# Optimization experiments

Hardware: AMD Instinct MI355X
Metric: run time of the kernel (lower is better)

## Reference

```python
import jax, jax.numpy as jnp
import numpy as np

MAX_DISP = 4  # pad_size == max_displacement per module validation
EPS = 1e-12   # torch F.normalize default eps


def _l2_normalize(x):
    # F.normalize(x) with default dim=1 (channels), p=2
    norm = jnp.sqrt(jnp.sum(x * x, axis=1, keepdims=True))
    return x / jnp.maximum(norm, EPS)


def setup_inputs() -> dict:
    key = jax.random.key(0)
    k1, k2 = jax.random.split(key)
    B, C, H, W = 8, 256, 96, 128
    fr = jax.random.normal(k1, (B, C, H, W), dtype=jnp.float32)
    fq = jax.random.normal(k2, (B, C, H, W), dtype=jnp.float32)
    return {"fr": fr, "fq": fq}


def reference(fr, fq):
    r = MAX_DISP
    H, W = fr.shape[2], fr.shape[3]
    frn = _l2_normalize(fr)
    # Normalization is per-pixel over channels, so normalize-then-pad equals
    # pad-then-normalize (padded zero columns stay zero under the eps clamp).
    fq_pad = jnp.pad(_l2_normalize(fq), ((0, 0), (0, 0), (r, r), (r, r)))
    # Offset order: dy (rows) outer, dx (cols) inner -> matches torch meshgrid 'ij' flatten.
    outs = [
        jnp.mean(frn * fq_pad[:, :, dy:H + dy, dx:W + dx], axis=1, keepdims=True)
        for dy in range(2 * r + 1)
        for dx in range(2 * r + 1)
    ]
    return jnp.concatenate(outs, axis=1)  # (B, (2r+1)^2, H, W)
```

## Files before the change

### kernel.cpp

```cpp
#include <hip/hip_runtime.h>


#define BB 8
#define CC 256
#define HH 96
#define WW 128
#define HW (HH*WW)
#define CHW (CC*HW)
#define NDISP 81
#define TYS 4
#define HX4 18
#define NSLOT (TYS*HX4)
#define CK 4
#define NCHK (CC/CK)
#define NST (NSLOT*CK)
#define YT (HH/TYS)
#define XT 2
#define NTILES (BB*YT*XT)
#define NGRP 9
#define EPSN 1e-12f

__device__ __forceinline__ void dma16(const void* g, void* l) {
    __builtin_amdgcn_global_load_lds(
        (const __attribute__((address_space(1))) void*)g,
        (__attribute__((address_space(3))) void*)l,
        16, 0, 0);
}

__global__ __launch_bounds__(64) __attribute__((amdgpu_waves_per_eu(4, 4)))
void corr_kernel(
    const float* __restrict__ fr, const float* __restrict__ fq,
    float* __restrict__ out)
{
    __shared__ float4 s_fq[2][NST];

    const int lane = threadIdx.x;
    const int tx   = lane & 15;
    const int ty   = lane >> 4;

    const int tile = blockIdx.x % NTILES;
    const int dy   = blockIdx.x / NTILES;
    const int b    = tile / (YT * XT);
    const int rem  = tile % (YT * XT);
    const int y0   = (rem >> 1) * TYS;
    const int x0   = (rem & 1) * 64;

    int soff[5];
#pragma unroll
    for (int j = 0; j < 5; ++j) {
        int i = 64 * j + lane;
        int c    = (i / NSLOT) & 3;
        int s    = i % NSLOT;
        int row  = s / HX4;
        int col4 = s % HX4;
        int gy = y0 + dy - 4 + row;
        int gx = x0 - 4 + col4 * 4;
        gy = min(max(gy, 0), HH - 1);
        gx = min(max(gx, 0), WW - 4);
        soff[j] = b * CHW + c * HW + gy * WW + gx;
    }

    const int frbase = b * CHW + (y0 + ty) * WW + x0 + tx * 4;

#pragma unroll
    for (int j = 0; j < 4; ++j)
        dma16(fq + soff[j], &s_fq[0][64 * j]);
    if (lane < 32)
        dma16(fq + soff[4], &s_fq[0][256]);

    float4 fra[CK];
#pragma unroll
    for (int c = 0; c < CK; ++c)
        fra[c] = *(const float4*)(fr + frbase + c * HW);

    float4 acc[9];
#pragma unroll
    for (int d = 0; d < 9; ++d) acc[d] = make_float4(0.f, 0.f, 0.f, 0.f);
    float sqn[12];
#pragma unroll
    for (int i = 0; i < 12; ++i) sqn[i] = 0.f;
    float4 fr2 = make_float4(0.f, 0.f, 0.f, 0.f);

#pragma unroll 1
    for (int ch = 0; ch < NCHK; ++ch) {
        const int p   = ch & 1;
        const int nch = (ch + 1 < NCHK) ? ch + 1 : ch;
        const int nco = nch * (CK * HW);

#pragma unroll
        for (int j = 0; j < 4; ++j)
            dma16(fq + soff[j] + nco, &s_fq[1 - p][64 * j]);
        if (lane < 32)
            dma16(fq + soff[4] + nco, &s_fq[1 - p][256]);

        __builtin_amdgcn_s_waitcnt(0x0F79);
        __builtin_amdgcn_sched_barrier(0);

#pragma unroll
        for (int c = 0; c < CK; ++c) {
            float4 a = fra[c];
            fra[c] = *(const float4*)(fr + frbase + nco + c * HW);
            fr2.x += a.x * a.x; fr2.y += a.y * a.y;
            fr2.z += a.z * a.z; fr2.w += a.w * a.w;

            float rw[12];
#pragma unroll
            for (int s4 = 0; s4 < 3; ++s4) {
                float4 t = s_fq[p][c * NSLOT + ty * HX4 + tx + s4];
                rw[s4 * 4 + 0] = t.x;
                rw[s4 * 4 + 1] = t.y;
                rw[s4 * 4 + 2] = t.z;
                rw[s4 * 4 + 3] = t.w;
            }
#pragma unroll
            for (int i = 0; i < 12; ++i) sqn[i] += rw[i] * rw[i];
#pragma unroll
            for (int dx = 0; dx < 9; ++dx) {
                acc[dx].x += a.x * rw[dx + 0];
                acc[dx].y += a.y * rw[dx + 1];
                acc[dx].z += a.z * rw[dx + 2];
                acc[dx].w += a.w * rw[dx + 3];
            }
        }
    }

    __builtin_amdgcn_s_waitcnt(0x0F70);

    float inq[12];
#pragma unroll
    for (int i = 0; i < 12; ++i)
        inq[i] = 1.0f / fmaxf(sqrtf(sqn[i]), EPSN);

    float4 ir;
    ir.x = 1.0f / fmaxf(sqrtf(fr2.x), EPSN);
    ir.y = 1.0f / fmaxf(sqrtf(fr2.y), EPSN);
    ir.z = 1.0f / fmaxf(sqrtf(fr2.z), EPSN);
    ir.w = 1.0f / fmaxf(sqrtf(fr2.w), EPSN);

    const bool rowok = ((unsigned)(y0 + ty + dy - 4) < (unsigned)HH);
    const int  xe0   = x0 + tx * 4;
    const float inv256 = 1.0f / 256.0f;
    const int obase = (b * NDISP + dy * 9) * HW + (y0 + ty) * WW + xe0;
#pragma unroll
    for (int dx = 0; dx < 9; ++dx) {
        float4 a = acc[dx];
        float4 o;
        o.x = a.x * ir.x * inq[dx + 0] * inv256;
        o.y = a.y * ir.y * inq[dx + 1] * inv256;
        o.z = a.z * ir.z * inq[dx + 2] * inv256;
        o.w = a.w * ir.w * inq[dx + 3] * inv256;
        const int cb = xe0 + dx - 4;
        o.x = (rowok && (unsigned)(cb    ) < (unsigned)WW) ? o.x : 0.f;
        o.y = (rowok && (unsigned)(cb + 1) < (unsigned)WW) ? o.y : 0.f;
        o.z = (rowok && (unsigned)(cb + 2) < (unsigned)WW) ? o.z : 0.f;
        o.w = (rowok && (unsigned)(cb + 3) < (unsigned)WW) ? o.w : 0.f;
        *(float4*)(out + obase + dx * HW) = o;
    }
}

extern "C" void kernel_launch(void* const* d_in, const int* in_sizes, int n_in,
                              void* d_out, int out_size, void* d_ws, size_t ws_size,
                              hipStream_t stream) {
    const float* fr = (const float*)d_in[0];
    const float* fq = (const float*)d_in[1];
    float* out = (float*)d_out;
    corr_kernel<<<dim3(NTILES * NGRP), dim3(64), 0, stream>>>(fr, fq, out);
}
```

Measured before the change: 326.8 us.

## Process three vertical displacements per block sharing a taller fq halo tile

```diff
diff --git a/kernel.cpp b/kernel.cpp
--- a/kernel.cpp
+++ b/kernel.cpp
@@ -9,15 +9,18 @@
 #define CHW (CC*HW)
 #define NDISP 81
 #define TYS 4
+#define GD 3
+#define HROWS (TYS+GD-1)
 #define HX4 18
-#define NSLOT (TYS*HX4)
+#define NSLOT (HROWS*HX4)
 #define CK 4
+#define CKHW (CK*HW)
 #define NCHK (CC/CK)
 #define NST (NSLOT*CK)
 #define YT (HH/TYS)
 #define XT 2
 #define NTILES (BB*YT*XT)
-#define NGRP 9
+#define NGRP 3
 #define EPSN 1e-12f
 
 __device__ __forceinline__ void dma16(const void* g, void* l) {
@@ -27,7 +30,7 @@
         16, 0, 0);
 }
 
-__global__ __launch_bounds__(64) __attribute__((amdgpu_waves_per_eu(4, 4)))
+__global__ __launch_bounds__(64) __attribute__((amdgpu_waves_per_eu(2, 8)))
 void corr_kernel(
     const float* __restrict__ fr, const float* __restrict__ fq,
     float* __restrict__ out)
@@ -39,21 +42,21 @@
     const int ty   = lane >> 4;
 
     const int tile = blockIdx.x % NTILES;
-    const int dy   = blockIdx.x / NTILES;
+    const int dyg  = blockIdx.x / NTILES;
     const int b    = tile / (YT * XT);
     const int rem  = tile % (YT * XT);
     const int y0   = (rem >> 1) * TYS;
     const int x0   = (rem & 1) * 64;
 
-    int soff[5];
+    int soff[7];
 #pragma unroll
-    for (int j = 0; j < 5; ++j) {
+    for (int j = 0; j < 7; ++j) {
         int i = 64 * j + lane;
         int c    = (i / NSLOT) & 3;
         int s    = i % NSLOT;
         int row  = s / HX4;
         int col4 = s % HX4;
-        int gy = y0 + dy - 4 + row;
+        int gy = y0 + 3 * dyg - 4 + row;
         int gx = x0 - 4 + col4 * 4;
         gy = min(max(gy, 0), HH - 1);
         gx = min(max(gx, 0), WW - 4);
@@ -63,37 +66,41 @@
     const int frbase = b * CHW + (y0 + ty) * WW + x0 + tx * 4;
 
 #pragma unroll
-    for (int j = 0; j < 4; ++j)
+    for (int j = 0; j < 6; ++j)
         dma16(fq + soff[j], &s_fq[0][64 * j]);
-    if (lane < 32)
-        dma16(fq + soff[4], &s_fq[0][256]);
+    if (lane < 48)
+        dma16(fq + soff[6], &s_fq[0][384]);
 
     float4 fra[CK];
 #pragma unroll
     for (int c = 0; c < CK; ++c)
         fra[c] = *(const float4*)(fr + frbase + c * HW);
 
-    float4 acc[9];
+    float4 acc[GD][9];
 #pragma unroll
-    for (int d = 0; d < 9; ++d) acc[d] = make_float4(0.f, 0.f, 0.f, 0.f);
-    float sqn[12];
+    for (int g = 0; g < GD; ++g)
 #pragma unroll
-    for (int i = 0; i < 12; ++i) sqn[i] = 0.f;
+        for (int d = 0; d < 9; ++d) acc[g][d] = make_float4(0.f, 0.f, 0.f, 0.f);
+    float sqn[GD][12];
+#pragma unroll
+    for (int g = 0; g < GD; ++g)
+#pragma unroll
+        for (int i = 0; i < 12; ++i) sqn[g][i] = 0.f;
     float4 fr2 = make_float4(0.f, 0.f, 0.f, 0.f);
 
 #pragma unroll 1
     for (int ch = 0; ch < NCHK; ++ch) {
         const int p   = ch & 1;
         const int nch = (ch + 1 < NCHK) ? ch + 1 : ch;
-        const int nco = nch * (CK * HW);
+        const int nco = nch * CKHW;
 
 #pragma unroll
-        for (int j = 0; j < 4; ++j)
+        for (int j = 0; j < 6; ++j)
             dma16(fq + soff[j] + nco, &s_fq[1 - p][64 * j]);
-        if (lane < 32)
-            dma16(fq + soff[4] + nco, &s_fq[1 - p][256]);
+        if (lane < 48)
+            dma16(fq + soff[6] + nco, &s_fq[1 - p][384]);
 
-        __builtin_amdgcn_s_waitcnt(0x0F79);
+        __builtin_amdgcn_s_waitcnt(0x0F7B);
         __builtin_amdgcn_sched_barrier(0);
 
 #pragma unroll
@@ -103,33 +110,31 @@
             fr2.x += a.x * a.x; fr2.y += a.y * a.y;
             fr2.z += a.z * a.z; fr2.w += a.w * a.w;
 
-            float rw[12];
 #pragma unroll
-            for (int s4 = 0; s4 < 3; ++s4) {
-                float4 t = s_fq[p][c * NSLOT + ty * HX4 + tx + s4];
-                rw[s4 * 4 + 0] = t.x;
-                rw[s4 * 4 + 1] = t.y;
-                rw[s4 * 4 + 2] = t.z;
-                rw[s4 * 4 + 3] = t.w;
-            }
+            for (int g = 0; g < GD; ++g) {
+                float rw[12];
 #pragma unroll
-            for (int i = 0; i < 12; ++i) sqn[i] += rw[i] * rw[i];
+                for (int s4 = 0; s4 < 3; ++s4) {
+                    float4 t = s_fq[p][c * NSLOT + (ty + g) * HX4 + tx + s4];
+                    rw[s4 * 4 + 0] = t.x;
+                    rw[s4 * 4 + 1] = t.y;
+                    rw[s4 * 4 + 2] = t.z;
+                    rw[s4 * 4 + 3] = t.w;
+                }
 #pragma unroll
-            for (int dx = 0; dx < 9; ++dx) {
-                acc[dx].x += a.x * rw[dx + 0];
-                acc[dx].y += a.y * rw[dx + 1];
-                acc[dx].z += a.z * rw[dx + 2];
-                acc[dx].w += a.w * rw[dx + 3];
+                for (int i = 0; i < 12; ++i) sqn[g][i] += rw[i] * rw[i];
+#pragma unroll
+                for (int dx = 0; dx < 9; ++dx) {
+                    acc[g][dx].x += a.x * rw[dx + 0];
+                    acc[g][dx].y += a.y * rw[dx + 1];
+                    acc[g][dx].z += a.z * rw[dx + 2];
+                    acc[g][dx].w += a.w * rw[dx + 3];
+                }
             }
         }
     }
 
     __builtin_amdgcn_s_waitcnt(0x0F70);
-
-    float inq[12];
-#pragma unroll
-    for (int i = 0; i < 12; ++i)
-        inq[i] = 1.0f / fmaxf(sqrtf(sqn[i]), EPSN);
 
     float4 ir;
     ir.x = 1.0f / fmaxf(sqrtf(fr2.x), EPSN);
@@ -137,24 +142,34 @@
     ir.z = 1.0f / fmaxf(sqrtf(fr2.z), EPSN);
     ir.w = 1.0f / fmaxf(sqrtf(fr2.w), EPSN);
 
-    const bool rowok = ((unsigned)(y0 + ty + dy - 4) < (unsigned)HH);
     const int  xe0   = x0 + tx * 4;
     const float inv256 = 1.0f / 256.0f;
-    const int obase = (b * NDISP + dy * 9) * HW + (y0 + ty) * WW + xe0;
+
 #pragma unroll
-    for (int dx = 0; dx < 9; ++dx) {
-        float4 a = acc[dx];
-        float4 o;
-        o.x = a.x * ir.x * inq[dx + 0] * inv256;
-        o.y = a.y * ir.y * inq[dx + 1] * inv256;
-        o.z = a.z * ir.z * inq[dx + 2] * inv256;
-        o.w = a.w * ir.w * inq[dx + 3] * inv256;
-        const int cb = xe0 + dx - 4;
-        o.x = (rowok && (unsigned)(cb    ) < (unsigned)WW) ? o.x : 0.f;
-        o.y = (rowok && (unsigned)(cb + 1) < (unsigned)WW) ? o.y : 0.f;
-        o.z = (rowok && (unsigned)(cb + 2) < (unsigned)WW) ? o.z : 0.f;
-        o.w = (rowok && (unsigned)(cb + 3) < (unsigned)WW) ? o.w : 0.f;
-        *(float4*)(out + obase + dx * HW) = o;
+    for (int g = 0; g < GD; ++g) {
+        const int dy = 3 * dyg + g;
+        float inq[12];
+#pragma unroll
+        for (int i = 0; i < 12; ++i)
+            inq[i] = 1.0f / fmaxf(sqrtf(sqn[g][i]), EPSN);
+
+        const bool rowok = ((unsigned)(y0 + ty + dy - 4) < (unsigned)HH);
+        const int obase = (b * NDISP + dy * 9) * HW + (y0 + ty) * WW + xe0;
+#pragma unroll
+        for (int dx = 0; dx < 9; ++dx) {
+            float4 a = acc[g][dx];
+            float4 o;
+            o.x = a.x * ir.x * inq[dx + 0] * inv256;
+            o.y = a.y * ir.y * inq[dx + 1] * inv256;
+            o.z = a.z * ir.z * inq[dx + 2] * inv256;
+            o.w = a.w * ir.w * inq[dx + 3] * inv256;
+            const int cb = xe0 + dx - 4;
+            o.x = (rowok && (unsigned)(cb    ) < (unsigned)WW) ? o.x : 0.f;
+            o.y = (rowok && (unsigned)(cb + 1) < (unsigned)WW) ? o.y : 0.f;
+            o.z = (rowok && (unsigned)(cb + 2) < (unsigned)WW) ? o.z : 0.f;
+            o.w = (rowok && (unsigned)(cb + 3) < (unsigned)WW) ? o.w : 0.f;
+            *(float4*)(out + obase + dx * HW) = o;
+        }
     }
 }
 
```

Result: faster. 284.8 us (-12.8%).
